# Kernel tuning notes

Measured on AMD Instinct MI355X. Metric: run time of the kernel, lower is better.

## Reference

```python
import jax, jax.numpy as jnp
import numpy as np

N_STREAMS = 4
DIM = 1024  # per-stream channels C
SINKHORN_ITERS = 50
SINKHORN_TAU = 0.1
RMS_EPS = 1.1920929e-07  # torch.finfo(float32).eps (nn.RMSNorm default eps=None)


def setup_inputs() -> dict:
    key = jax.random.key(0)
    ks = jax.random.split(key, 6)
    B, T = 4, 2048
    n, C = N_STREAMS, DIM
    wd = n * C  # widened_dim
    x = jax.random.normal(ks[0], (B, T, wd), dtype=jnp.float32)
    # projection weights, init std=0.01 (stored as [out, in] like nn.Linear)
    W_res = 0.01 * jax.random.normal(ks[1], (n * n, wd), dtype=jnp.float32)
    W_pre = 0.01 * jax.random.normal(ks[2], (n, wd), dtype=jnp.float32)
    W_post = 0.01 * jax.random.normal(ks[3], (n, wd), dtype=jnp.float32)
    # base logits
    H_res_base = jnp.full((n, n), -0.5, dtype=jnp.float32)
    H_res_base = H_res_base.at[jnp.arange(n), jnp.arange(n)].set(0.0)
    H_pre_base = jnp.zeros((n,), dtype=jnp.float32).at[0].set(1.0)
    H_post_base = jnp.zeros((n,), dtype=jnp.float32)
    gate = jnp.array([5.0], dtype=jnp.float32)
    # branch_fn stand-in: single C->C linear
    W_branch = (1.0 / np.sqrt(C)) * jax.random.normal(ks[4], (C, C), dtype=jnp.float32)
    return {"x": x, "W_res": W_res, "W_pre": W_pre, "W_post": W_post,
            "H_res_base": H_res_base, "H_pre_base": H_pre_base,
            "H_post_base": H_post_base, "gate": gate, "W_branch": W_branch}


def sinkhorn_log(logits, num_iters=SINKHORN_ITERS, tau=SINKHORN_TAU):
    # logits: [..., n, n]
    Z = logits / tau
    u0 = jnp.zeros(Z.shape[:-1], Z.dtype)  # [..., n]
    v0 = jnp.zeros_like(u0)

    def step(carry, _):
        u, v = carry
        u = -jax.nn.logsumexp(Z + v[..., None, :], axis=-1)
        v = -jax.nn.logsumexp(Z + u[..., :, None], axis=-2)
        return (u, v), None

    (u, v), _ = jax.lax.scan(step, (u0, v0), None, length=num_iters)
    return jnp.exp(Z + u[..., :, None] + v[..., None, :])


def reference(x, W_res, W_pre, W_post, H_res_base, H_pre_base, H_post_base, gate, W_branch):
    B, T, nC = x.shape
    n = N_STREAMS
    C = nC // n
    # RMSNorm (no affine)
    x_norm = x * jax.lax.rsqrt(jnp.mean(x * x, axis=-1, keepdims=True) + RMS_EPS)
    # projections (Linear stores [out, in])
    H_res_logits = (x_norm @ W_res.T).reshape(B, T, n, n) + H_res_base
    H_pre_logits = x_norm @ W_pre.T + H_pre_base
    H_post_logits = x_norm @ W_post.T + H_post_base
    H_res = sinkhorn_log(H_res_logits)
    H_pre = jax.nn.softmax(H_pre_logits, axis=-1)
    H_post = jax.nn.softmax(H_post_logits, axis=-1)
    g = jax.nn.sigmoid(gate)[0]  # eval mode: no exploration noise
    I = jnp.eye(n, dtype=H_res.dtype)
    H_res = (1.0 - g) * I + g * H_res
    x_streams = x.reshape(B, T, n, C)
    x_pre = jnp.einsum('btnc,btn->btc', x_streams, H_pre)
    y = x_pre @ W_branch  # branch_fn stand-in
    x_mixed = jnp.einsum('btij,btjc->btic', H_res, x_streams)
    y_distributed = jnp.einsum('btc,btn->btnc', y, H_post)
    return (x_mixed + y_distributed).reshape(B, T, nC)
```

## Files before the change

### kernel.cpp

```cpp
#include <hip/hip_runtime.h>
#include <cstdint>
#include <cstddef>

#define NTOK 8192
#define WD   4096
#define CD   1024
#define EPS_RMS 1.1920929e-07f
#define TAU_INV 10.0f

using half8  = __attribute__((ext_vector_type(8))) _Float16;
using half4v = __attribute__((ext_vector_type(4))) _Float16;
using f32x4  = __attribute__((ext_vector_type(4))) float;

__global__ __launch_bounds__(256) void k_wt(const float* __restrict__ W,
                                            _Float16* __restrict__ WT) {
  __shared__ float tile[64][65];
  const int t  = threadIdx.x;
  const int c0 = (blockIdx.x & 15) * 64;
  const int k0 = (blockIdx.x >> 4) * 64;
  const int a = t & 63, b = t >> 6;
#pragma unroll
  for (int i = 0; i < 16; ++i) {
    int k = b + i * 4;
    tile[k][a] = W[(size_t)(k0 + k) * CD + (c0 + a)];
  }
  __syncthreads();
#pragma unroll
  for (int i = 0; i < 16; ++i) {
    int c = b + i * 4;
    WT[(size_t)(c0 + c) * CD + (k0 + a)] = (_Float16)tile[a][c];
  }
}

__global__ __launch_bounds__(256) void k_wcat(const float* __restrict__ Wres,
                                              const float* __restrict__ Wpre,
                                              const float* __restrict__ Wpost,
                                              _Float16* __restrict__ Wcat) {
  const int id  = blockIdx.x * 256 + threadIdx.x;
  const int row = id >> 10;
  const int kq  = id & 1023;
  float4 v = make_float4(0.f, 0.f, 0.f, 0.f);
  if (row < 16)      v = *(const float4*)(Wres + (size_t)row * WD + kq * 4);
  else if (row < 20) v = *(const float4*)(Wpre + (size_t)(row - 16) * WD + kq * 4);
  else if (row < 24) v = *(const float4*)(Wpost + (size_t)(row - 20) * WD + kq * 4);
  half4v h;
  h[0] = (_Float16)v.x; h[1] = (_Float16)v.y; h[2] = (_Float16)v.z; h[3] = (_Float16)v.w;
  *(half4v*)(Wcat + (size_t)row * WD + kq * 4) = h;
}

#define LDA 72
__global__ __launch_bounds__(512, 4) void k_stats3(
    const float* __restrict__ x, const _Float16* __restrict__ Wcat,
    const float* __restrict__ baseRes, const float* __restrict__ basePre,
    const float* __restrict__ basePost, const float* __restrict__ gate,
    float* __restrict__ HpostOut, float* __restrict__ HresF,
    _Float16* __restrict__ xpre)
{
  __shared__ _Float16 As[2][4][16 * LDA];
  __shared__ _Float16 Bs[2][4][32 * LDA];
  __shared__ float Lpart[4][16][32];
  __shared__ float ssPart[4][16];
  __shared__ float invS[16];
  __shared__ float HpreS[16][4];

  const int t    = threadIdx.x;
  const int lane = t & 63;
  const int wid  = t >> 6;
  const int p    = wid >> 1;
  const int g    = wid & 1;
  const int tp   = t & 127;
  const int tok0 = blockIdx.x * 16;
  const int fr   = lane & 15, kg = lane >> 4;

  const int ar = tp >> 4;
  const int ak = (tp & 15) * 4;
  const int br = tp >> 3;
  const int bk = (tp & 7) * 8;
  const int Kb = p * 1024;

  f32x4 acc = {0.f, 0.f, 0.f, 0.f};
  float ss0 = 0.f, ss1 = 0.f;

  const float* xa0 = x + (size_t)(tok0 + ar) * WD + Kb + ak;
  const float* xa1 = x + (size_t)(tok0 + ar + 8) * WD + Kb + ak;
  const _Float16* wb0 = Wcat + (size_t)br * WD + Kb + bk;
  const _Float16* wb1 = Wcat + (size_t)(br + 16) * WD + Kb + bk;

  float4 a0 = *(const float4*)(xa0);
  float4 a1 = *(const float4*)(xa1);
  half8 b0 = *(const half8*)(wb0);
  half8 b1 = *(const half8*)(wb1);
  {
    ss0 += a0.x * a0.x + a0.y * a0.y + a0.z * a0.z + a0.w * a0.w;
    ss1 += a1.x * a1.x + a1.y * a1.y + a1.z * a1.z + a1.w * a1.w;
    half4v h0, h1;
    h0[0] = (_Float16)a0.x; h0[1] = (_Float16)a0.y; h0[2] = (_Float16)a0.z; h0[3] = (_Float16)a0.w;
    h1[0] = (_Float16)a1.x; h1[1] = (_Float16)a1.y; h1[2] = (_Float16)a1.z; h1[3] = (_Float16)a1.w;
    *(half4v*)&As[0][p][ar * LDA + ak] = h0;
    *(half4v*)&As[0][p][(ar + 8) * LDA + ak] = h1;
    *(half8*)&Bs[0][p][br * LDA + bk] = b0;
    *(half8*)&Bs[0][p][(br + 16) * LDA + bk] = b1;
  }
  __syncthreads();

  int cur = 0;
  for (int kt = 0; kt < 16; ++kt) {
    if (kt < 15) {
      const int ko = (kt + 1) * 64;
      a0 = *(const float4*)(xa0 + ko);
      a1 = *(const float4*)(xa1 + ko);
      b0 = *(const half8*)(wb0 + ko);
      b1 = *(const half8*)(wb1 + ko);
    }
    half8 af0 = *(const half8*)&As[cur][p][fr * LDA + kg * 8];
    half8 af1 = *(const half8*)&As[cur][p][fr * LDA + 32 + kg * 8];
    half8 bf0 = *(const half8*)&Bs[cur][p][(g * 16 + fr) * LDA + kg * 8];
    half8 bf1 = *(const half8*)&Bs[cur][p][(g * 16 + fr) * LDA + 32 + kg * 8];
    acc = __builtin_amdgcn_mfma_f32_16x16x32_f16(af0, bf0, acc, 0, 0, 0);
    acc = __builtin_amdgcn_mfma_f32_16x16x32_f16(af1, bf1, acc, 0, 0, 0);
    if (kt < 15) {
      ss0 += a0.x * a0.x + a0.y * a0.y + a0.z * a0.z + a0.w * a0.w;
      ss1 += a1.x * a1.x + a1.y * a1.y + a1.z * a1.z + a1.w * a1.w;
      half4v h0, h1;
      h0[0] = (_Float16)a0.x; h0[1] = (_Float16)a0.y; h0[2] = (_Float16)a0.z; h0[3] = (_Float16)a0.w;
      h1[0] = (_Float16)a1.x; h1[1] = (_Float16)a1.y; h1[2] = (_Float16)a1.z; h1[3] = (_Float16)a1.w;
      *(half4v*)&As[cur ^ 1][p][ar * LDA + ak] = h0;
      *(half4v*)&As[cur ^ 1][p][(ar + 8) * LDA + ak] = h1;
      *(half8*)&Bs[cur ^ 1][p][br * LDA + bk] = b0;
      *(half8*)&Bs[cur ^ 1][p][(br + 16) * LDA + bk] = b1;
    }
    __syncthreads();
    cur ^= 1;
  }

#define QR(v) { v += __shfl_xor(v, 1); v += __shfl_xor(v, 2); \
                v += __shfl_xor(v, 4); v += __shfl_xor(v, 8); }
  QR(ss0) QR(ss1)
#undef QR
  if ((tp & 15) == 0) { ssPart[p][ar] = ss0; ssPart[p][ar + 8] = ss1; }

#pragma unroll
  for (int r = 0; r < 4; ++r) Lpart[p][kg * 4 + r][g * 16 + fr] = acc[r];
  __syncthreads();

  if (t < 16) {
    const float s = ssPart[0][t] + ssPart[1][t] + ssPart[2][t] + ssPart[3][t];
    const float inv = rsqrtf(s * (1.0f / (float)WD) + EPS_RMS);
    invS[t] = inv;
    float pr[4], q[4];
#pragma unroll
    for (int j = 0; j < 4; ++j) {
      const float lp = Lpart[0][t][16 + j] + Lpart[1][t][16 + j] +
                       Lpart[2][t][16 + j] + Lpart[3][t][16 + j];
      pr[j] = fmaf(lp, inv, basePre[j]);
      const float lq = Lpart[0][t][20 + j] + Lpart[1][t][20 + j] +
                       Lpart[2][t][20 + j] + Lpart[3][t][20 + j];
      q[j] = fmaf(lq, inv, basePost[j]);
    }
    {
      const float m = fmaxf(fmaxf(pr[0], pr[1]), fmaxf(pr[2], pr[3]));
      float s2 = 0.f;
#pragma unroll
      for (int j = 0; j < 4; ++j) { pr[j] = __expf(pr[j] - m); s2 += pr[j]; }
      const float rs = 1.0f / s2;
#pragma unroll
      for (int j = 0; j < 4; ++j) HpreS[t][j] = pr[j] * rs;
    }
    {
      const float m = fmaxf(fmaxf(q[0], q[1]), fmaxf(q[2], q[3]));
      float s2 = 0.f;
#pragma unroll
      for (int j = 0; j < 4; ++j) { q[j] = __expf(q[j] - m); s2 += q[j]; }
      const float rs = 1.0f / s2;
      float4 qv; qv.x = q[0] * rs; qv.y = q[1] * rs; qv.z = q[2] * rs; qv.w = q[3] * rs;
      *(float4*)(HpostOut + (size_t)(tok0 + t) * 4) = qv;
    }
  }
  __syncthreads();

  if (t < 256) {
    const int tk  = t >> 4;
    const int l16 = t & 15;
    const float Lsum = Lpart[0][tk][l16] + Lpart[1][tk][l16] +
                       Lpart[2][tk][l16] + Lpart[3][tk][l16];
    const float Z = fmaf(Lsum, invS[tk], baseRes[l16]) * TAU_INV;
    const int i = l16 >> 2, j = l16 & 3;
    float u = 0.0f, v = 0.0f;
    for (int itr = 0; itr < 50; ++itr) {
      float a = Z + v;
      float m = fmaxf(a, __shfl_xor(a, 1)); m = fmaxf(m, __shfl_xor(m, 2));
      float s = __expf(a - m);
      s += __shfl_xor(s, 1); s += __shfl_xor(s, 2);
      u = -(m + __logf(s));
      float b = Z + u;
      float m2 = fmaxf(b, __shfl_xor(b, 4)); m2 = fmaxf(m2, __shfl_xor(m2, 8));
      float s2 = __expf(b - m2);
      s2 += __shfl_xor(s2, 4); s2 += __shfl_xor(s2, 8);
      v = -(m2 + __logf(s2));
    }
    const float H = __expf(Z + u + v);
    const float gg = 1.0f / (1.0f + __expf(-gate[0]));
    HresF[(size_t)(tok0 + tk) * 16 + l16] = gg * H + ((i == j) ? (1.0f - gg) : 0.0f);
  } else {
    const int q16 = (t - 256) >> 4;
    const int l16 = t & 15;
    const int tok = tok0 + q16;
    const float p0 = HpreS[q16][0], p1 = HpreS[q16][1];
    const float p2 = HpreS[q16][2], p3 = HpreS[q16][3];
    const float* xr = x + (size_t)tok * WD;
    _Float16* xp = xpre + (size_t)tok * CD;
#pragma unroll 2
    for (int it = 0; it < 16; ++it) {
      const int c4 = it * 64 + l16 * 4;
      const float4 s0 = *(const float4*)(xr + c4);
      const float4 s1 = *(const float4*)(xr + CD + c4);
      const float4 s2 = *(const float4*)(xr + 2 * CD + c4);
      const float4 s3 = *(const float4*)(xr + 3 * CD + c4);
      half4v h;
      h[0] = (_Float16)(p0 * s0.x + p1 * s1.x + p2 * s2.x + p3 * s3.x);
      h[1] = (_Float16)(p0 * s0.y + p1 * s1.y + p2 * s2.y + p3 * s3.y);
      h[2] = (_Float16)(p0 * s0.z + p1 * s1.z + p2 * s2.z + p3 * s3.z);
      h[3] = (_Float16)(p0 * s0.w + p1 * s1.w + p2 * s2.w + p3 * s3.w);
      *(half4v*)(xp + c4) = h;
    }
  }
}

#define LDK 72
__global__ __launch_bounds__(256, 2) void k_gemm_epi(
    const _Float16* __restrict__ xpre, const _Float16* __restrict__ WT,
    const float* __restrict__ x, const float* __restrict__ HresF,
    const float* __restrict__ Hpost, float* __restrict__ out)
{
  __shared__ _Float16 As[128 * LDK];
  __shared__ _Float16 Bs[128 * LDK];
  const int tid  = threadIdx.x;
  const int nb   = blockIdx.x & 7;
  const int mb   = blockIdx.x >> 3;
  const int tok0 = mb * 128;
  const int cb   = nb * 128;
  const int lane = tid & 63, wid = tid >> 6;
  const int wr = (wid >> 1) * 64, wc = (wid & 1) * 64;
  const int fr = lane & 15, kg = lane >> 4;

  f32x4 acc[4][4];
#pragma unroll
  for (int m = 0; m < 4; ++m)
#pragma unroll
    for (int n = 0; n < 4; ++n) { f32x4 z = {0.f, 0.f, 0.f, 0.f}; acc[m][n] = z; }

  for (int kt = 0; kt < 16; ++kt) {
#pragma unroll
    for (int i = 0; i < 4; ++i) {
      const int chunk = tid + i * 256;
      const int r = chunk >> 3;
      const int ko = (chunk & 7) * 8;
      *(half8*)&As[r * LDK + ko] =
          *(const half8*)&xpre[(size_t)(tok0 + r) * CD + kt * 64 + ko];
      *(half8*)&Bs[r * LDK + ko] =
          *(const half8*)&WT[(size_t)(cb + r) * CD + kt * 64 + ko];
    }
    __syncthreads();
#pragma unroll
    for (int kk = 0; kk < 2; ++kk) {
      half8 a[4], b[4];
#pragma unroll
      for (int m = 0; m < 4; ++m)
        a[m] = *(const half8*)&As[(wr + m * 16 + fr) * LDK + kk * 32 + kg * 8];
#pragma unroll
      for (int n = 0; n < 4; ++n)
        b[n] = *(const half8*)&Bs[(wc + n * 16 + fr) * LDK + kk * 32 + kg * 8];
#pragma unroll
      for (int m = 0; m < 4; ++m)
#pragma unroll
        for (int n = 0; n < 4; ++n)
          acc[m][n] = __builtin_amdgcn_mfma_f32_16x16x32_f16(a[m], b[n], acc[m][n], 0, 0, 0);
    }
    __syncthreads();
  }

  float* Hs = (float*)As;
  for (int idx = tid; idx < 128 * 20; idx += 256) {
    const int tl = idx / 20, e = idx % 20;
    Hs[idx] = (e < 16) ? HresF[(size_t)(tok0 + tl) * 16 + e]
                       : Hpost[(size_t)(tok0 + tl) * 4 + (e - 16)];
  }
  __syncthreads();

#pragma unroll
  for (int m = 0; m < 4; ++m) {
#pragma unroll
    for (int reg = 0; reg < 4; ++reg) {
      const int tl = wr + m * 16 + (lane >> 4) * 4 + reg;
      const size_t trow = (size_t)(tok0 + tl) * WD;
      float H[20];
#pragma unroll
      for (int e = 0; e < 20; ++e) H[e] = Hs[tl * 20 + e];
#pragma unroll
      for (int n = 0; n < 4; ++n) {
        const int c = cb + wc + n * 16 + (lane & 15);
        const float yv = acc[m][n][reg];
        const float x0 = x[trow + c];
        const float x1 = x[trow + CD + c];
        const float x2 = x[trow + 2 * CD + c];
        const float x3 = x[trow + 3 * CD + c];
#pragma unroll
        for (int i = 0; i < 4; ++i) {
          out[trow + i * CD + c] =
              H[i * 4 + 0] * x0 + H[i * 4 + 1] * x1 + H[i * 4 + 2] * x2 +
              H[i * 4 + 3] * x3 + H[16 + i] * yv;
        }
      }
    }
  }
}

extern "C" void kernel_launch(void* const* d_in, const int* in_sizes, int n_in,
                              void* d_out, int out_size, void* d_ws, size_t ws_size,
                              hipStream_t stream) {
  const float* x        = (const float*)d_in[0];
  const float* Wres     = (const float*)d_in[1];
  const float* Wpre     = (const float*)d_in[2];
  const float* Wpost    = (const float*)d_in[3];
  const float* baseRes  = (const float*)d_in[4];
  const float* basePre  = (const float*)d_in[5];
  const float* basePost = (const float*)d_in[6];
  const float* gate     = (const float*)d_in[7];
  const float* Wb       = (const float*)d_in[8];
  float* out = (float*)d_out;

  char* ws = (char*)d_ws;
  _Float16* xpre  = (_Float16*)(ws);
  _Float16* WT    = (_Float16*)(ws + 16777216);
  float*    HresF = (float*)(ws + 19398656);
  float*    Hpst  = (float*)(ws + 19922944);
  _Float16* Wcat  = (_Float16*)(ws + 20054016);

  k_wt<<<256, 256, 0, stream>>>(Wb, WT);
  k_wcat<<<128, 256, 0, stream>>>(Wres, Wpre, Wpost, Wcat);
  k_stats3<<<512, 512, 0, stream>>>(x, Wcat, baseRes, basePre, basePost, gate,
                                    Hpst, HresF, xpre);
  k_gemm_epi<<<512, 256, 0, stream>>>(xpre, WT, x, HresF, Hpst, out);
}
```

Before: 128.0 us.

## Load stats-GEMM operands straight into MFMA registers and merge prep kernels

The stats kernel drops its LDS double-buffered staging and __syncthreads per K step. Each of 8 waves now reads x and Wcat straight from global memory into MFMA operand registers over its own 512-wide K chunk, computing both 16-column output halves. Partial results are reduced across 8 waves in shared memory instead of 4. The two weight-prep kernels are also merged into one launch. This removes LDS traffic and barrier stalls in exchange for less coalesced global loads and a larger cross-wave reduction.

```diff
diff --git a/kernel.cpp b/kernel.cpp
--- a/kernel.cpp
+++ b/kernel.cpp
@@ -12,150 +12,114 @@
 using half4v = __attribute__((ext_vector_type(4))) _Float16;
 using f32x4  = __attribute__((ext_vector_type(4))) float;
 
-__global__ __launch_bounds__(256) void k_wt(const float* __restrict__ W,
-                                            _Float16* __restrict__ WT) {
-  __shared__ float tile[64][65];
-  const int t  = threadIdx.x;
-  const int c0 = (blockIdx.x & 15) * 64;
-  const int k0 = (blockIdx.x >> 4) * 64;
-  const int a = t & 63, b = t >> 6;
-#pragma unroll
-  for (int i = 0; i < 16; ++i) {
-    int k = b + i * 4;
-    tile[k][a] = W[(size_t)(k0 + k) * CD + (c0 + a)];
-  }
-  __syncthreads();
-#pragma unroll
-  for (int i = 0; i < 16; ++i) {
-    int c = b + i * 4;
-    WT[(size_t)(c0 + c) * CD + (k0 + a)] = (_Float16)tile[a][c];
-  }
-}
-
-__global__ __launch_bounds__(256) void k_wcat(const float* __restrict__ Wres,
+__global__ __launch_bounds__(256) void k_prep(const float* __restrict__ W,
+                                              _Float16* __restrict__ WT,
+                                              const float* __restrict__ Wres,
                                               const float* __restrict__ Wpre,
                                               const float* __restrict__ Wpost,
                                               _Float16* __restrict__ Wcat) {
-  const int id  = blockIdx.x * 256 + threadIdx.x;
-  const int row = id >> 10;
-  const int kq  = id & 1023;
-  float4 v = make_float4(0.f, 0.f, 0.f, 0.f);
-  if (row < 16)      v = *(const float4*)(Wres + (size_t)row * WD + kq * 4);
-  else if (row < 20) v = *(const float4*)(Wpre + (size_t)(row - 16) * WD + kq * 4);
-  else if (row < 24) v = *(const float4*)(Wpost + (size_t)(row - 20) * WD + kq * 4);
-  half4v h;
-  h[0] = (_Float16)v.x; h[1] = (_Float16)v.y; h[2] = (_Float16)v.z; h[3] = (_Float16)v.w;
-  *(half4v*)(Wcat + (size_t)row * WD + kq * 4) = h;
+  if (blockIdx.x < 256) {
+    __shared__ float tile[64][65];
+    const int t  = threadIdx.x;
+    const int c0 = (blockIdx.x & 15) * 64;
+    const int k0 = (blockIdx.x >> 4) * 64;
+    const int a = t & 63, b = t >> 6;
+#pragma unroll
+    for (int i = 0; i < 16; ++i) {
+      int k = b + i * 4;
+      tile[k][a] = W[(size_t)(k0 + k) * CD + (c0 + a)];
+    }
+    __syncthreads();
+#pragma unroll
+    for (int i = 0; i < 16; ++i) {
+      int c = b + i * 4;
+      WT[(size_t)(c0 + c) * CD + (k0 + a)] = (_Float16)tile[a][c];
+    }
+  } else {
+    const int id  = (blockIdx.x - 256) * 256 + threadIdx.x;
+    const int row = id >> 10;
+    const int kq  = id & 1023;
+    float4 v = make_float4(0.f, 0.f, 0.f, 0.f);
+    if (row < 16)      v = *(const float4*)(Wres + (size_t)row * WD + kq * 4);
+    else if (row < 20) v = *(const float4*)(Wpre + (size_t)(row - 16) * WD + kq * 4);
+    else if (row < 24) v = *(const float4*)(Wpost + (size_t)(row - 20) * WD + kq * 4);
+    half4v h;
+    h[0] = (_Float16)v.x; h[1] = (_Float16)v.y; h[2] = (_Float16)v.z; h[3] = (_Float16)v.w;
+    *(half4v*)(Wcat + (size_t)row * WD + kq * 4) = h;
+  }
 }
 
-#define LDA 72
-__global__ __launch_bounds__(512, 4) void k_stats3(
+#define KCH 512
+__global__ __launch_bounds__(512, 6) void k_stats4(
     const float* __restrict__ x, const _Float16* __restrict__ Wcat,
     const float* __restrict__ baseRes, const float* __restrict__ basePre,
     const float* __restrict__ basePost, const float* __restrict__ gate,
     float* __restrict__ HpostOut, float* __restrict__ HresF,
     _Float16* __restrict__ xpre)
 {
-  __shared__ _Float16 As[2][4][16 * LDA];
-  __shared__ _Float16 Bs[2][4][32 * LDA];
-  __shared__ float Lpart[4][16][32];
-  __shared__ float ssPart[4][16];
+  __shared__ float Lpart[8][16][32];
+  __shared__ float ssPart[8][16];
   __shared__ float invS[16];
   __shared__ float HpreS[16][4];
 
   const int t    = threadIdx.x;
   const int lane = t & 63;
-  const int wid  = t >> 6;
-  const int p    = wid >> 1;
-  const int g    = wid & 1;
-  const int tp   = t & 127;
+  const int p    = t >> 6;
   const int tok0 = blockIdx.x * 16;
   const int fr   = lane & 15, kg = lane >> 4;
 
-  const int ar = tp >> 4;
-  const int ak = (tp & 15) * 4;
-  const int br = tp >> 3;
-  const int bk = (tp & 7) * 8;
-  const int Kb = p * 1024;
-
-  f32x4 acc = {0.f, 0.f, 0.f, 0.f};
-  float ss0 = 0.f, ss1 = 0.f;
-
-  const float* xa0 = x + (size_t)(tok0 + ar) * WD + Kb + ak;
-  const float* xa1 = x + (size_t)(tok0 + ar + 8) * WD + Kb + ak;
-  const _Float16* wb0 = Wcat + (size_t)br * WD + Kb + bk;
-  const _Float16* wb1 = Wcat + (size_t)(br + 16) * WD + Kb + bk;
-
-  float4 a0 = *(const float4*)(xa0);
-  float4 a1 = *(const float4*)(xa1);
-  half8 b0 = *(const half8*)(wb0);
-  half8 b1 = *(const half8*)(wb1);
-  {
-    ss0 += a0.x * a0.x + a0.y * a0.y + a0.z * a0.z + a0.w * a0.w;
-    ss1 += a1.x * a1.x + a1.y * a1.y + a1.z * a1.z + a1.w * a1.w;
-    half4v h0, h1;
-    h0[0] = (_Float16)a0.x; h0[1] = (_Float16)a0.y; h0[2] = (_Float16)a0.z; h0[3] = (_Float16)a0.w;
-    h1[0] = (_Float16)a1.x; h1[1] = (_Float16)a1.y; h1[2] = (_Float16)a1.z; h1[3] = (_Float16)a1.w;
-    *(half4v*)&As[0][p][ar * LDA + ak] = h0;
-    *(half4v*)&As[0][p][(ar + 8) * LDA + ak] = h1;
-    *(half8*)&Bs[0][p][br * LDA + bk] = b0;
-    *(half8*)&Bs[0][p][(br + 16) * LDA + bk] = b1;
+  const float*    xr = x    + (size_t)(tok0 + fr) * WD + p * KCH + kg * 8;
+  const _Float16* w0 = Wcat + (size_t)fr * WD        + p * KCH + kg * 8;
+  const _Float16* w1 = Wcat + (size_t)(16 + fr) * WD + p * KCH + kg * 8;
+
+  f32x4 acc0 = {0.f, 0.f, 0.f, 0.f};
+  f32x4 acc1 = {0.f, 0.f, 0.f, 0.f};
+  float ss = 0.f;
+
+#pragma unroll
+  for (int kt = 0; kt < 16; ++kt) {
+    const int ko = kt * 32;
+    const float4 u = *(const float4*)(xr + ko);
+    const float4 v = *(const float4*)(xr + ko + 4);
+    const half8 b0 = *(const half8*)(w0 + ko);
+    const half8 b1 = *(const half8*)(w1 + ko);
+    ss += u.x * u.x + u.y * u.y + u.z * u.z + u.w * u.w;
+    ss += v.x * v.x + v.y * v.y + v.z * v.z + v.w * v.w;
+    half8 a;
+    a[0] = (_Float16)u.x; a[1] = (_Float16)u.y; a[2] = (_Float16)u.z; a[3] = (_Float16)u.w;
+    a[4] = (_Float16)v.x; a[5] = (_Float16)v.y; a[6] = (_Float16)v.z; a[7] = (_Float16)v.w;
+    acc0 = __builtin_amdgcn_mfma_f32_16x16x32_f16(a, b0, acc0, 0, 0, 0);
+    acc1 = __builtin_amdgcn_mfma_f32_16x16x32_f16(a, b1, acc1, 0, 0, 0);
+  }
+
+  ss += __shfl_xor(ss, 16);
+  ss += __shfl_xor(ss, 32);
+  if (lane < 16) ssPart[p][lane] = ss;
+
+#pragma unroll
+  for (int r = 0; r < 4; ++r) {
+    Lpart[p][kg * 4 + r][fr]      = acc0[r];
+    Lpart[p][kg * 4 + r][16 + fr] = acc1[r];
   }
   __syncthreads();
 
-  int cur = 0;
-  for (int kt = 0; kt < 16; ++kt) {
-    if (kt < 15) {
-      const int ko = (kt + 1) * 64;
-      a0 = *(const float4*)(xa0 + ko);
-      a1 = *(const float4*)(xa1 + ko);
-      b0 = *(const half8*)(wb0 + ko);
-      b1 = *(const half8*)(wb1 + ko);
-    }
-    half8 af0 = *(const half8*)&As[cur][p][fr * LDA + kg * 8];
-    half8 af1 = *(const half8*)&As[cur][p][fr * LDA + 32 + kg * 8];
-    half8 bf0 = *(const half8*)&Bs[cur][p][(g * 16 + fr) * LDA + kg * 8];
-    half8 bf1 = *(const half8*)&Bs[cur][p][(g * 16 + fr) * LDA + 32 + kg * 8];
-    acc = __builtin_amdgcn_mfma_f32_16x16x32_f16(af0, bf0, acc, 0, 0, 0);
-    acc = __builtin_amdgcn_mfma_f32_16x16x32_f16(af1, bf1, acc, 0, 0, 0);
-    if (kt < 15) {
-      ss0 += a0.x * a0.x + a0.y * a0.y + a0.z * a0.z + a0.w * a0.w;
-      ss1 += a1.x * a1.x + a1.y * a1.y + a1.z * a1.z + a1.w * a1.w;
-      half4v h0, h1;
-      h0[0] = (_Float16)a0.x; h0[1] = (_Float16)a0.y; h0[2] = (_Float16)a0.z; h0[3] = (_Float16)a0.w;
-      h1[0] = (_Float16)a1.x; h1[1] = (_Float16)a1.y; h1[2] = (_Float16)a1.z; h1[3] = (_Float16)a1.w;
-      *(half4v*)&As[cur ^ 1][p][ar * LDA + ak] = h0;
-      *(half4v*)&As[cur ^ 1][p][(ar + 8) * LDA + ak] = h1;
-      *(half8*)&Bs[cur ^ 1][p][br * LDA + bk] = b0;
-      *(half8*)&Bs[cur ^ 1][p][(br + 16) * LDA + bk] = b1;
-    }
-    __syncthreads();
-    cur ^= 1;
-  }
-
-#define QR(v) { v += __shfl_xor(v, 1); v += __shfl_xor(v, 2); \
-                v += __shfl_xor(v, 4); v += __shfl_xor(v, 8); }
-  QR(ss0) QR(ss1)
-#undef QR
-  if ((tp & 15) == 0) { ssPart[p][ar] = ss0; ssPart[p][ar + 8] = ss1; }
-
-#pragma unroll
-  for (int r = 0; r < 4; ++r) Lpart[p][kg * 4 + r][g * 16 + fr] = acc[r];
-  __syncthreads();
-
   if (t < 16) {
-    const float s = ssPart[0][t] + ssPart[1][t] + ssPart[2][t] + ssPart[3][t];
+    float s = 0.f;
+#pragma unroll
+    for (int pp = 0; pp < 8; ++pp) s += ssPart[pp][t];
     const float inv = rsqrtf(s * (1.0f / (float)WD) + EPS_RMS);
     invS[t] = inv;
     float pr[4], q[4];
 #pragma unroll
     for (int j = 0; j < 4; ++j) {
-      const float lp = Lpart[0][t][16 + j] + Lpart[1][t][16 + j] +
-                       Lpart[2][t][16 + j] + Lpart[3][t][16 + j];
+      float lp = 0.f, lq = 0.f;
+#pragma unroll
+      for (int pp = 0; pp < 8; ++pp) {
+        lp += Lpart[pp][t][16 + j];
+        lq += Lpart[pp][t][20 + j];
+      }
       pr[j] = fmaf(lp, inv, basePre[j]);
-      const float lq = Lpart[0][t][20 + j] + Lpart[1][t][20 + j] +
-                       Lpart[2][t][20 + j] + Lpart[3][t][20 + j];
-      q[j] = fmaf(lq, inv, basePost[j]);
+      q[j]  = fmaf(lq, inv, basePost[j]);
     }
     {
       const float m = fmaxf(fmaxf(pr[0], pr[1]), fmaxf(pr[2], pr[3]));
@@ -181,8 +145,9 @@
   if (t < 256) {
     const int tk  = t >> 4;
     const int l16 = t & 15;
-    const float Lsum = Lpart[0][tk][l16] + Lpart[1][tk][l16] +
-                       Lpart[2][tk][l16] + Lpart[3][tk][l16];
+    float Lsum = 0.f;
+#pragma unroll
+    for (int pp = 0; pp < 8; ++pp) Lsum += Lpart[pp][tk][l16];
     const float Z = fmaf(Lsum, invS[tk], baseRes[l16]) * TAU_INV;
     const int i = l16 >> 2, j = l16 & 3;
     float u = 0.0f, v = 0.0f;
@@ -207,15 +172,15 @@
     const int tok = tok0 + q16;
     const float p0 = HpreS[q16][0], p1 = HpreS[q16][1];
     const float p2 = HpreS[q16][2], p3 = HpreS[q16][3];
-    const float* xr = x + (size_t)tok * WD;
+    const float* xrow = x + (size_t)tok * WD;
     _Float16* xp = xpre + (size_t)tok * CD;
 #pragma unroll 2
     for (int it = 0; it < 16; ++it) {
       const int c4 = it * 64 + l16 * 4;
-      const float4 s0 = *(const float4*)(xr + c4);
-      const float4 s1 = *(const float4*)(xr + CD + c4);
-      const float4 s2 = *(const float4*)(xr + 2 * CD + c4);
-      const float4 s3 = *(const float4*)(xr + 3 * CD + c4);
+      const float4 s0 = *(const float4*)(xrow + c4);
+      const float4 s1 = *(const float4*)(xrow + CD + c4);
+      const float4 s2 = *(const float4*)(xrow + 2 * CD + c4);
+      const float4 s3 = *(const float4*)(xrow + 3 * CD + c4);
       half4v h;
       h[0] = (_Float16)(p0 * s0.x + p1 * s1.x + p2 * s2.x + p3 * s3.x);
       h[1] = (_Float16)(p0 * s0.y + p1 * s1.y + p2 * s2.y + p3 * s3.y);
@@ -336,9 +301,8 @@
   float*    Hpst  = (float*)(ws + 19922944);
   _Float16* Wcat  = (_Float16*)(ws + 20054016);
 
-  k_wt<<<256, 256, 0, stream>>>(Wb, WT);
-  k_wcat<<<128, 256, 0, stream>>>(Wres, Wpre, Wpost, Wcat);
-  k_stats3<<<512, 512, 0, stream>>>(x, Wcat, baseRes, basePre, basePost, gate,
+  k_prep<<<384, 256, 0, stream>>>(Wb, WT, Wres, Wpre, Wpost, Wcat);
+  k_stats4<<<512, 512, 0, stream>>>(x, Wcat, baseRes, basePre, basePost, gate,
                                     Hpst, HresF, xpre);
   k_gemm_epi<<<512, 256, 0, stream>>>(xpre, WT, x, HresF, Hpst, out);
 }
```

Result: slower. 140.7 us (+10.0%).
